# Kernel tuning notes

Measured on AMD Instinct MI355X. Metric: run time of the kernel, lower is better.

## Reference

```python
import jax, jax.numpy as jnp
import numpy as np

B, S, E, H = 4, 2048, 1024, 16
K = 9           # number of boundaries per batch (K-1 = 8 passages)
DH = E // H


def make_relevance_mask(boundaries, relevance_scores, seq_len):
    """Vectorized equivalent of the Python-loop mask builder.

    boundaries: (B, K) int, sorted; boundaries[:,0] == q_end.
    relevance_scores: (B, K-1) float.
    Returns float mask (B, S, S) with values {0, 1, relevance}.
    """
    Bsz, Kb = boundaries.shape
    idx = jnp.arange(seq_len, dtype=boundaries.dtype)
    # pid[b, s] = j s.t. boundaries[b, j] <= s < boundaries[b, j+1]; -1 before b[0]
    pid = jax.vmap(lambda bb: jnp.searchsorted(bb, idx, side='right'))(boundaries) - 1  # (B,S)
    in_pass = (pid >= 0) & (pid < Kb - 1)  # inside some passage span
    rel_g = jnp.take_along_axis(relevance_scores, jnp.clip(pid, 0, Kb - 2), axis=1)  # (B,S)
    # query rows (pos < q_end): columns in passage j -> relevance[j], else 1
    col_val = jnp.where(in_pass, rel_g, 1.0)  # (B,S)
    qrow = idx[None, :] < boundaries[:, :1]   # (B,S)
    # non-query rows: 1 iff same passage block, else 0
    same = in_pass[:, :, None] & in_pass[:, None, :] & (pid[:, :, None] == pid[:, None, :])
    mask = jnp.where(qrow[:, :, None], col_val[:, None, :], jnp.where(same, 1.0, 0.0))
    return mask.astype(jnp.float32)


def setup_inputs() -> dict:
    key = jax.random.key(0)
    k1, k2, k3, k4, k5, k6, k7 = jax.random.split(key, 7)
    hidden_states = jax.random.normal(k1, (B, S, E), dtype=jnp.float32)
    relevance_scores = jax.random.uniform(k2, (B, K - 1), dtype=jnp.float32)
    passage_boundaries = jnp.sort(jax.random.randint(k3, (B, K), 0, S, dtype=jnp.int32), axis=1)
    in_proj_w = 0.02 * jax.random.normal(k4, (3 * E, E), dtype=jnp.float32)
    in_proj_b = jnp.zeros((3 * E,), dtype=jnp.float32)
    out_w = 0.02 * jax.random.normal(k5, (E, E), dtype=jnp.float32)
    out_b = jnp.zeros((E,), dtype=jnp.float32)
    return {
        'hidden_states': hidden_states,
        'relevance_scores': relevance_scores,
        'passage_boundaries': passage_boundaries,
        'in_proj_w': in_proj_w,
        'in_proj_b': in_proj_b,
        'out_w': out_w,
        'out_b': out_b,
    }


def reference(hidden_states, relevance_scores, passage_boundaries,
              in_proj_w, in_proj_b, out_w, out_b):
    Bsz, Sl, Em = hidden_states.shape
    mask = make_relevance_mask(passage_boundaries, relevance_scores, Sl)  # (B,S,S)
    qkv = hidden_states @ in_proj_w.T + in_proj_b              # (B,S,3E)
    q, k, v = jnp.split(qkv, 3, axis=-1)
    def heads(t):
        return t.reshape(Bsz, Sl, H, DH).transpose(0, 2, 1, 3)  # (B,H,S,Dh)
    q, k, v = heads(q), heads(k), heads(v)
    scale = 1.0 / jnp.sqrt(jnp.float32(DH))
    scores = jnp.einsum('bhqd,bhkd->bhqk', q * scale, k) + mask[:, None]  # float mask is ADDED
    attn = jax.nn.softmax(scores, axis=-1)
    out = jnp.einsum('bhqk,bhkd->bhqd', attn, v)
    out = out.transpose(0, 2, 1, 3).reshape(Bsz, Sl, Em)
    return out @ out_w.T + out_b
```

## Files before the change

kernel.cpp:

```cpp
#include <hip/hip_runtime.h>
#include <math.h>

#define Bsz 4
#define Sq  2048
#define Eq  1024
#define Hh  16
#define DHd 64
#define Kb  9
#define GSTR 72
#define LOG2E 1.44269504088896340736f
#define NCLS 10

typedef _Float16 f16;
typedef __attribute__((ext_vector_type(8))) _Float16 fh8;
typedef __attribute__((ext_vector_type(4))) _Float16 fh4;
typedef __attribute__((ext_vector_type(2))) _Float16 fh2;
typedef __attribute__((ext_vector_type(4))) float fx4;
typedef __attribute__((ext_vector_type(16))) float fx16;
typedef __attribute__((ext_vector_type(4))) int i4;

#define SWZ(r, c) ((r) * 64 + ((c) ^ (((r) & 7) << 3)))

static __device__ __forceinline__ float fexp2(float x) {
#if __has_builtin(__builtin_amdgcn_exp2f)
  return __builtin_amdgcn_exp2f(x);
#else
  return __expf(x * 0.6931471805599453f);
#endif
}

__global__ void pid_kernel(const int* __restrict__ bnd, const float* __restrict__ rel,
                           int* __restrict__ pidr, float* __restrict__ lfTab) {
  int idx = blockIdx.x * blockDim.x + threadIdx.x;
  if (idx >= Bsz * Sq) return;
  int b = idx >> 11;
  int s = idx & (Sq - 1);
  int j = -1;
#pragma unroll
  for (int t = 0; t < Kb; ++t) {
    if (bnd[b * Kb + t] <= s) j = t;
  }
  pidr[idx] = j;
  bool inp = (j >= 0 && j < Kb - 1);
  float cv = inp ? rel[b * (Kb - 1) + j] : 1.0f;
  float* base = &lfTab[(size_t)b * NCLS * Sq + s];
  base[0] = cv * LOG2E;
#pragma unroll
  for (int c = 1; c < NCLS; ++c)
    base[c * Sq] = (inp && j == c - 1) ? LOG2E : 0.0f;
}

__global__ __launch_bounds__(256) void cvt_hs(const float* __restrict__ x,
                                              f16* __restrict__ xo) {
  int i = (blockIdx.x * blockDim.x + threadIdx.x) * 8;
  float4 a = *(const float4*)&x[i];
  float4 b = *(const float4*)&x[i + 4];
  fh8 o;
  o[0] = (f16)a.x; o[1] = (f16)a.y; o[2] = (f16)a.z; o[3] = (f16)a.w;
  o[4] = (f16)b.x; o[5] = (f16)b.y; o[6] = (f16)b.z; o[7] = (f16)b.w;
  *(fh8*)&xo[i] = o;
}

template <int MODE>
__global__ __launch_bounds__(256) void gemm_f16(
    const f16* __restrict__ A, const float* __restrict__ Bf,
    const float* __restrict__ bias, float* __restrict__ Cp,
    int M, int N, int Kd,
    f16* __restrict__ qo, f16* __restrict__ ko, f16* __restrict__ vto) {
  __shared__ __align__(16) f16 Ash[128 * GSTR];
  __shared__ __align__(16) f16 Bsh[128 * GSTR];

  const int tid = threadIdx.x;
  const int lane = tid & 63, w = tid >> 6;
  const int wm = w >> 1, wn = w & 1;
  const int q16 = lane & 15, quad = lane >> 4;
  const int m_blk = blockIdx.y * 128, n_blk = blockIdx.x * 128;

  fx4 acc[4][4];
#pragma unroll
  for (int mt = 0; mt < 4; ++mt)
#pragma unroll
    for (int nt = 0; nt < 4; ++nt)
#pragma unroll
      for (int r = 0; r < 4; ++r) acc[mt][nt][r] = 0.f;

  const int sr = tid >> 2, sc = (tid & 3) * 16;

  for (int k0 = 0; k0 < Kd; k0 += 64) {
    __syncthreads();
#pragma unroll
    for (int h = 0; h < 2; ++h) {
      const int r = sr + h * 64;
      const f16* ga = &A[(size_t)(m_blk + r) * Kd + k0 + sc];
      *(fh8*)&Ash[r * GSTR + sc]     = *(const fh8*)&ga[0];
      *(fh8*)&Ash[r * GSTR + sc + 8] = *(const fh8*)&ga[8];
      const float* gb = &Bf[(size_t)(n_blk + r) * Kd + k0 + sc];
      float4 f0 = *(const float4*)&gb[0];
      float4 f1 = *(const float4*)&gb[4];
      float4 f2 = *(const float4*)&gb[8];
      float4 f3 = *(const float4*)&gb[12];
      fh8 b0, b1;
      b0[0] = (f16)f0.x; b0[1] = (f16)f0.y; b0[2] = (f16)f0.z; b0[3] = (f16)f0.w;
      b0[4] = (f16)f1.x; b0[5] = (f16)f1.y; b0[6] = (f16)f1.z; b0[7] = (f16)f1.w;
      b1[0] = (f16)f2.x; b1[1] = (f16)f2.y; b1[2] = (f16)f2.z; b1[3] = (f16)f2.w;
      b1[4] = (f16)f3.x; b1[5] = (f16)f3.y; b1[6] = (f16)f3.z; b1[7] = (f16)f3.w;
      *(fh8*)&Bsh[r * GSTR + sc]     = b0;
      *(fh8*)&Bsh[r * GSTR + sc + 8] = b1;
    }
    __syncthreads();

#pragma unroll
    for (int ks = 0; ks < 2; ++ks) {
      fh8 af[4], bfr[4];
#pragma unroll
      for (int mt = 0; mt < 4; ++mt)
        af[mt] = *(const fh8*)&Ash[(wm * 64 + mt * 16 + q16) * GSTR + ks * 32 + quad * 8];
#pragma unroll
      for (int nt = 0; nt < 4; ++nt)
        bfr[nt] = *(const fh8*)&Bsh[(wn * 64 + nt * 16 + q16) * GSTR + ks * 32 + quad * 8];
#pragma unroll
      for (int nt = 0; nt < 4; ++nt)
#pragma unroll
        for (int mt = 0; mt < 4; ++mt)
          acc[mt][nt] = __builtin_amdgcn_mfma_f32_16x16x32_f16(af[mt], bfr[nt], acc[mt][nt], 0, 0, 0);
    }
  }

  float bsv[4];
#pragma unroll
  for (int nt = 0; nt < 4; ++nt) bsv[nt] = bias[n_blk + wn * 64 + nt * 16 + q16];

  if (MODE == 0) {
#pragma unroll
    for (int mt = 0; mt < 4; ++mt)
#pragma unroll
      for (int r = 0; r < 4; ++r) {
        int row = m_blk + wm * 64 + mt * 16 + quad * 4 + r;
#pragma unroll
        for (int nt = 0; nt < 4; ++nt) {
          int col = n_blk + wn * 64 + nt * 16 + q16;
          Cp[(size_t)row * N + col] = acc[mt][nt][r] + bsv[nt];
        }
      }
  } else {
    const int n0 = n_blk + wn * 64;
    const int which = n0 >> 10;
    const int hd = (n0 & 1023) >> 6;
    const float scale = (which == 0) ? 0.125f * LOG2E : 1.0f;
#pragma unroll
    for (int mt = 0; mt < 4; ++mt)
#pragma unroll
      for (int r = 0; r < 4; ++r) {
        int m = m_blk + wm * 64 + mt * 16 + quad * 4 + r;
        int b = m >> 11, s = m & (Sq - 1);
#pragma unroll
        for (int nt = 0; nt < 4; ++nt) {
          int d = nt * 16 + q16;
          float x = (acc[mt][nt][r] + bsv[nt]) * scale;
          if (which == 2) {
            vto[(((size_t)(b * Hh + hd)) * DHd + d) * Sq + s] = (f16)x;
          } else {
            f16* dst = (which == 0) ? qo : ko;
            dst[(((size_t)(b * Hh + hd)) * Sq + s) * DHd + d] = (f16)x;
          }
        }
      }
  }
}

__global__ __launch_bounds__(256, 2) void attn_v4(
    const f16* __restrict__ Qf, const f16* __restrict__ Kf,
    const f16* __restrict__ Vt, const int* __restrict__ pidr,
    const float* __restrict__ lfTab, f16* __restrict__ attf) {
  const int qb = blockIdx.x, hd = blockIdx.y, b = blockIdx.z;
  const int bh = b * Hh + hd;
  const int tid = threadIdx.x;
  const int lane = tid & 63, w = tid >> 6;
  const int l31 = lane & 31, hi = lane >> 5;

  __shared__ __align__(16) f16 Ks[2][64 * 64];
  __shared__ __align__(16) f16 Vs[2][64 * 64];

  const size_t qkbase = (size_t)bh * Sq * DHd;
  const size_t vtbase = (size_t)bh * DHd * Sq;
  const int qrow = qb * 128 + w * 32 + l31;

  fh8 qf[4];
  {
    const f16* qp = &Qf[qkbase + (size_t)qrow * DHd + hi * 8];
#pragma unroll
    for (int ds = 0; ds < 4; ++ds) qf[ds] = *(const fh8*)&qp[ds * 16];
  }

  const int rq = pidr[b * Sq + qrow];
  const float* lfrow = &lfTab[((size_t)(b * NCLS + (rq + 1))) * Sq + 4 * hi];

  fh8 onesf;
#pragma unroll
  for (int j = 0; j < 8; ++j) onesf[j] = (l31 == 0) ? (f16)1.0f : (f16)0.0f;

  fx16 o_acc[2], lacc;
#pragma unroll
  for (int r = 0; r < 16; ++r) { o_acc[0][r] = 0.f; o_acc[1][r] = 0.f; lacc[r] = 0.f; }

  const int sr = tid >> 2, sc = (tid & 3) * 16;
  const int NT = Sq / 64;

  fh8 kc0, kc1, vc0, vc1;
  {
    const f16* gk = &Kf[qkbase + (size_t)sr * DHd + sc];
    kc0 = *(const fh8*)&gk[0]; kc1 = *(const fh8*)&gk[8];
    const f16* gv = &Vt[vtbase + (size_t)sr * Sq + sc];
    vc0 = *(const fh8*)&gv[0]; vc1 = *(const fh8*)&gv[8];
  }
  *(fh8*)&Ks[0][SWZ(sr, sc)]     = kc0;
  *(fh8*)&Ks[0][SWZ(sr, sc + 8)] = kc1;
  *(fh8*)&Vs[0][SWZ(sr, sc)]     = vc0;
  *(fh8*)&Vs[0][SWZ(sr, sc + 8)] = vc1;
  {
    const f16* gk = &Kf[qkbase + (size_t)(64 + sr) * DHd + sc];
    kc0 = *(const fh8*)&gk[0]; kc1 = *(const fh8*)&gk[8];
    const f16* gv = &Vt[vtbase + (size_t)sr * Sq + 64 + sc];
    vc0 = *(const fh8*)&gv[0]; vc1 = *(const fh8*)&gv[8];
  }
  __syncthreads();

  fx16 sacc0, sacc1;

  for (int kt = 0; kt < NT; ++kt) {
    const int c = kt & 1;

    {
      const float* lp = &lfrow[kt * 64];
#pragma unroll
      for (int g = 0; g < 4; ++g) {
        float4 a = *(const float4*)&lp[8 * g];
        sacc0[4 * g + 0] = a.x; sacc0[4 * g + 1] = a.y;
        sacc0[4 * g + 2] = a.z; sacc0[4 * g + 3] = a.w;
      }
    }

    if (kt + 1 < NT) {
      *(fh8*)&Ks[c ^ 1][SWZ(sr, sc)]     = kc0;
      *(fh8*)&Ks[c ^ 1][SWZ(sr, sc + 8)] = kc1;
      *(fh8*)&Vs[c ^ 1][SWZ(sr, sc)]     = vc0;
      *(fh8*)&Vs[c ^ 1][SWZ(sr, sc + 8)] = vc1;
      if (kt + 2 < NT) {
        const f16* gk = &Kf[qkbase + (size_t)((kt + 2) * 64 + sr) * DHd + sc];
        kc0 = *(const fh8*)&gk[0]; kc1 = *(const fh8*)&gk[8];
        const f16* gv = &Vt[vtbase + (size_t)sr * Sq + (kt + 2) * 64 + sc];
        vc0 = *(const fh8*)&gv[0]; vc1 = *(const fh8*)&gv[8];
      }
    }

    auto half = [&](fx16& sacc, int s, bool preload_next) {
      fh8 kfr[4];
#pragma unroll
      for (int ds = 0; ds < 4; ++ds)
        kfr[ds] = *(const fh8*)&Ks[c][SWZ(s * 32 + l31, ds * 16 + hi * 8)];
#pragma unroll
      for (int ds = 0; ds < 4; ++ds)
        sacc = __builtin_amdgcn_mfma_f32_32x32x16_f16(kfr[ds], qf[ds], sacc, 0, 0, 0);

      if (preload_next) {
        const float* lp = &lfrow[kt * 64 + 32];
#pragma unroll
        for (int g = 0; g < 4; ++g) {
          float4 a = *(const float4*)&lp[8 * g];
          sacc1[4 * g + 0] = a.x; sacc1[4 * g + 1] = a.y;
          sacc1[4 * g + 2] = a.z; sacc1[4 * g + 3] = a.w;
        }
      }

      int pk[8];
#pragma unroll
      for (int i = 0; i < 8; ++i) {
        fh2 h;
        h[0] = (f16)fexp2(sacc[2 * i]);
        h[1] = (f16)fexp2(sacc[2 * i + 1]);
        pk[i] = __builtin_bit_cast(int, h);
      }

      fh8 vfr[2][2];
#pragma unroll
      for (int dt = 0; dt < 2; ++dt)
#pragma unroll
        for (int kb = 0; kb < 2; ++kb)
          vfr[dt][kb] = *(const fh8*)&Vs[c][SWZ(dt * 32 + l31, s * 32 + kb * 16 + hi * 8)];

#pragma unroll
      for (int kb = 0; kb < 2; ++kb) {
        int a01 = pk[4 * kb + 0], a23 = pk[4 * kb + 1];
        int a45 = pk[4 * kb + 2], a67 = pk[4 * kb + 3];
        i4 t;
#if __has_builtin(__builtin_amdgcn_permlane32_swap)
        auto s0 = __builtin_amdgcn_permlane32_swap(a01, a45, false, false);
        auto s1 = __builtin_amdgcn_permlane32_swap(a23, a67, false, false);
        t[0] = s0[0]; t[1] = s1[0]; t[2] = s0[1]; t[3] = s1[1];
#else
        int x01 = __shfl_xor(a01, 32), x23 = __shfl_xor(a23, 32);
        int x45 = __shfl_xor(a45, 32), x67 = __shfl_xor(a67, 32);
        t[0] = hi ? x45 : a01; t[1] = hi ? x67 : a23;
        t[2] = hi ? a45 : x01; t[3] = hi ? a67 : x23;
#endif
        fh8 pf = __builtin_bit_cast(fh8, t);
        lacc = __builtin_amdgcn_mfma_f32_32x32x16_f16(onesf, pf, lacc, 0, 0, 0);
        o_acc[0] = __builtin_amdgcn_mfma_f32_32x32x16_f16(vfr[0][kb], pf, o_acc[0], 0, 0, 0);
        o_acc[1] = __builtin_amdgcn_mfma_f32_32x32x16_f16(vfr[1][kb], pf, o_acc[1], 0, 0, 0);
      }
    };

    half(sacc0, 0, true);
    half(sacc1, 1, false);

    if (kt + 1 < NT) __syncthreads();
  }

  float l = __shfl(lacc[0], l31);
  float inv = 1.0f / l;
  size_t obase = ((size_t)(b * Sq + qrow)) * Eq + hd * 64 + 4 * hi;
#pragma unroll
  for (int dt = 0; dt < 2; ++dt)
#pragma unroll
    for (int g = 0; g < 4; ++g) {
      fh4 o4;
#pragma unroll
      for (int j = 0; j < 4; ++j) o4[j] = (f16)(o_acc[dt][4 * g + j] * inv);
      *(fh4*)&attf[obase + dt * 32 + 8 * g] = o4;
    }
}

extern "C" void kernel_launch(void* const* d_in, const int* in_sizes, int n_in,
                              void* d_out, int out_size, void* d_ws, size_t ws_size,
                              hipStream_t stream) {
  const float* hs = (const float*)d_in[0];
  const float* rel = (const float*)d_in[1];
  const int* bnd = (const int*)d_in[2];
  const float* wi = (const float*)d_in[3];
  const float* bi = (const float*)d_in[4];
  const float* wo = (const float*)d_in[5];
  const float* bo = (const float*)d_in[6];
  float* out = (float*)d_out;

  const size_t NQ = (size_t)Bsz * Hh * Sq * DHd;
  char* p = (char*)d_ws;
  f16* qf = (f16*)p;   p += NQ * 2;
  f16* kf = (f16*)p;   p += NQ * 2;
  f16* vt = (f16*)p;   p += NQ * 2;
  f16* hsf = (f16*)p;  p += NQ * 2;
  f16* attf = (f16*)p; p += NQ * 2;
  int* pidr = (int*)p; p += Bsz * Sq * 4;
  float* lfTab = (float*)p;

  hipLaunchKernelGGL(pid_kernel, dim3((Bsz * Sq + 255) / 256), dim3(256), 0, stream,
                     bnd, rel, pidr, lfTab);
  hipLaunchKernelGGL(cvt_hs, dim3((int)(NQ / 8 / 256)), dim3(256), 0, stream,
                     hs, hsf);
  hipLaunchKernelGGL((gemm_f16<1>), dim3(24, 64), dim3(256), 0, stream,
                     hsf, wi, bi, (float*)nullptr, Bsz * Sq, 3 * Eq, Eq,
                     qf, kf, vt);
  hipLaunchKernelGGL(attn_v4, dim3(16, 16, 4), dim3(256), 0, stream,
                     qf, kf, vt, pidr, lfTab, attf);
  hipLaunchKernelGGL((gemm_f16<0>), dim3(8, 64), dim3(256), 0, stream,
                     attf, wo, bo, out, Bsz * Sq, Eq, Eq,
                     nullptr, nullptr, nullptr);
}
```

Measured before the change: 333.3 us.

## Pre-convert weights to f16, register-prefetch GEMM tiles, swizzle shared memory

```diff
diff --git a/kernel.cpp b/kernel.cpp
--- a/kernel.cpp
+++ b/kernel.cpp
@@ -7,7 +7,6 @@
 #define Hh  16
 #define DHd 64
 #define Kb  9
-#define GSTR 72
 #define LOG2E 1.44269504088896340736f
 #define NCLS 10
 
@@ -63,12 +62,12 @@
 
 template <int MODE>
 __global__ __launch_bounds__(256) void gemm_f16(
-    const f16* __restrict__ A, const float* __restrict__ Bf,
+    const f16* __restrict__ A, const f16* __restrict__ Bh,
     const float* __restrict__ bias, float* __restrict__ Cp,
     int M, int N, int Kd,
     f16* __restrict__ qo, f16* __restrict__ ko, f16* __restrict__ vto) {
-  __shared__ __align__(16) f16 Ash[128 * GSTR];
-  __shared__ __align__(16) f16 Bsh[128 * GSTR];
+  __shared__ __align__(16) f16 Ash[128 * 64];
+  __shared__ __align__(16) f16 Bsh[128 * 64];
 
   const int tid = threadIdx.x;
   const int lane = tid & 63, w = tid >> 6;
@@ -86,26 +85,41 @@
 
   const int sr = tid >> 2, sc = (tid & 3) * 16;
 
+  fh8 pa[2][2], pb[2][2];
+  const f16* ga0 = &A[(size_t)(m_blk + sr) * Kd + sc];
+  const f16* gb0 = &Bh[(size_t)(n_blk + sr) * Kd + sc];
+
+#pragma unroll
+  for (int h = 0; h < 2; ++h) {
+    const f16* ga = ga0 + (size_t)h * 64 * Kd;
+    pa[h][0] = *(const fh8*)&ga[0];
+    pa[h][1] = *(const fh8*)&ga[8];
+    const f16* gb = gb0 + (size_t)h * 64 * Kd;
+    pb[h][0] = *(const fh8*)&gb[0];
+    pb[h][1] = *(const fh8*)&gb[8];
+  }
+
   for (int k0 = 0; k0 < Kd; k0 += 64) {
     __syncthreads();
 #pragma unroll
     for (int h = 0; h < 2; ++h) {
       const int r = sr + h * 64;
-      const f16* ga = &A[(size_t)(m_blk + r) * Kd + k0 + sc];
-      *(fh8*)&Ash[r * GSTR + sc]     = *(const fh8*)&ga[0];
-      *(fh8*)&Ash[r * GSTR + sc + 8] = *(const fh8*)&ga[8];
-      const float* gb = &Bf[(size_t)(n_blk + r) * Kd + k0 + sc];
-      float4 f0 = *(const float4*)&gb[0];
-      float4 f1 = *(const float4*)&gb[4];
-      float4 f2 = *(const float4*)&gb[8];
-      float4 f3 = *(const float4*)&gb[12];
-      fh8 b0, b1;
-      b0[0] = (f16)f0.x; b0[1] = (f16)f0.y; b0[2] = (f16)f0.z; b0[3] = (f16)f0.w;
-      b0[4] = (f16)f1.x; b0[5] = (f16)f1.y; b0[6] = (f16)f1.z; b0[7] = (f16)f1.w;
-      b1[0] = (f16)f2.x; b1[1] = (f16)f2.y; b1[2] = (f16)f2.z; b1[3] = (f16)f2.w;
-      b1[4] = (f16)f3.x; b1[5] = (f16)f3.y; b1[6] = (f16)f3.z; b1[7] = (f16)f3.w;
-      *(fh8*)&Bsh[r * GSTR + sc]     = b0;
-      *(fh8*)&Bsh[r * GSTR + sc + 8] = b1;
+      *(fh8*)&Ash[SWZ(r, sc)]     = pa[h][0];
+      *(fh8*)&Ash[SWZ(r, sc + 8)] = pa[h][1];
+      *(fh8*)&Bsh[SWZ(r, sc)]     = pb[h][0];
+      *(fh8*)&Bsh[SWZ(r, sc + 8)] = pb[h][1];
+    }
+    if (k0 + 64 < Kd) {
+      const int kn = k0 + 64;
+#pragma unroll
+      for (int h = 0; h < 2; ++h) {
+        const f16* ga = ga0 + (size_t)h * 64 * Kd + kn;
+        pa[h][0] = *(const fh8*)&ga[0];
+        pa[h][1] = *(const fh8*)&ga[8];
+        const f16* gb = gb0 + (size_t)h * 64 * Kd + kn;
+        pb[h][0] = *(const fh8*)&gb[0];
+        pb[h][1] = *(const fh8*)&gb[8];
+      }
     }
     __syncthreads();
 
@@ -114,10 +128,10 @@
       fh8 af[4], bfr[4];
 #pragma unroll
       for (int mt = 0; mt < 4; ++mt)
-        af[mt] = *(const fh8*)&Ash[(wm * 64 + mt * 16 + q16) * GSTR + ks * 32 + quad * 8];
+        af[mt] = *(const fh8*)&Ash[SWZ(wm * 64 + mt * 16 + q16, ks * 32 + quad * 8)];
 #pragma unroll
       for (int nt = 0; nt < 4; ++nt)
-        bfr[nt] = *(const fh8*)&Bsh[(wn * 64 + nt * 16 + q16) * GSTR + ks * 32 + quad * 8];
+        bfr[nt] = *(const fh8*)&Bsh[SWZ(wn * 64 + nt * 16 + q16, ks * 32 + quad * 8)];
 #pragma unroll
       for (int nt = 0; nt < 4; ++nt)
 #pragma unroll
@@ -349,19 +363,22 @@
   f16* vt = (f16*)p;   p += NQ * 2;
   f16* hsf = (f16*)p;  p += NQ * 2;
   f16* attf = (f16*)p; p += NQ * 2;
+  f16* wif = (f16*)p;  p += (size_t)3 * Eq * Eq * 2;
+  f16* wof = (f16*)p;  p += (size_t)Eq * Eq * 2;
   int* pidr = (int*)p; p += Bsz * Sq * 4;
   float* lfTab = (float*)p;
 
   hipLaunchKernelGGL(pid_kernel, dim3((Bsz * Sq + 255) / 256), dim3(256), 0, stream,
                      bnd, rel, pidr, lfTab);
-  hipLaunchKernelGGL(cvt_hs, dim3((int)(NQ / 8 / 256)), dim3(256), 0, stream,
-                     hs, hsf);
+  hipLaunchKernelGGL(cvt_hs, dim3((int)(NQ / 2048)), dim3(256), 0, stream, hs, hsf);
+  hipLaunchKernelGGL(cvt_hs, dim3(3 * Eq * Eq / 2048), dim3(256), 0, stream, wi, wif);
+  hipLaunchKernelGGL(cvt_hs, dim3(Eq * Eq / 2048), dim3(256), 0, stream, wo, wof);
   hipLaunchKernelGGL((gemm_f16<1>), dim3(24, 64), dim3(256), 0, stream,
-                     hsf, wi, bi, (float*)nullptr, Bsz * Sq, 3 * Eq, Eq,
+                     hsf, wif, bi, (float*)nullptr, Bsz * Sq, 3 * Eq, Eq,
                      qf, kf, vt);
   hipLaunchKernelGGL(attn_v4, dim3(16, 16, 4), dim3(256), 0, stream,
                      qf, kf, vt, pidr, lfTab, attf);
   hipLaunchKernelGGL((gemm_f16<0>), dim3(8, 64), dim3(256), 0, stream,
-                     attf, wo, bo, out, Bsz * Sq, Eq, Eq,
+                     attf, wof, bo, out, Bsz * Sq, Eq, Eq,
                      nullptr, nullptr, nullptr);
 }
```

Measured after the change: 312.1 us. 6.4% less time.
